# Kernel optimization log

Measured on AMD Instinct MI355X. Metric: run time of the kernel, lower is better.

Reference implementation:

```python
import jax, jax.numpy as jnp
import numpy as np

B, T, I, H, L, O = 256, 2048, 64, 128, 2, 10


def setup_inputs() -> dict:
    key = jax.random.key(0)
    ks = jax.random.split(key, 12)
    s_i = 1.0 / np.sqrt(H)  # torch RNN init scale
    inp = {"x": jax.random.normal(ks[0], (B, T, I), dtype=jnp.float32)}
    in_sizes = [I, H]
    for l in range(L):
        inp[f"W_ih_{l}"] = jax.random.uniform(ks[1 + 4 * l], (3 * H, in_sizes[l]), minval=-s_i, maxval=s_i)
        inp[f"W_hh_{l}"] = jax.random.uniform(ks[2 + 4 * l], (3 * H, H), minval=-s_i, maxval=s_i)
        inp[f"b_ih_{l}"] = jax.random.uniform(ks[3 + 4 * l], (3 * H,), minval=-s_i, maxval=s_i)
        inp[f"b_hh_{l}"] = jax.random.uniform(ks[4 + 4 * l], (3 * H,), minval=-s_i, maxval=s_i)
    s_o = 1.0 / np.sqrt(H)
    inp["fc_W"] = jax.random.uniform(ks[9], (O, H), minval=-s_o, maxval=s_o)
    inp["fc_b"] = jax.random.uniform(ks[10], (O,), minval=-s_o, maxval=s_o)
    return inp


def gru_layer(x_seq, W_ih, W_hh, b_ih, b_hh):
    # x_seq: [B, T, D_in] -> hs: [B, T, H]. PyTorch GRU gate order: r, z, n.
    b, t, _ = x_seq.shape
    h = W_hh.shape[1]
    gates_x = jnp.einsum('bti,gi->btg', x_seq, W_ih) + b_ih  # [B, T, 3H], precomputed

    def step(h_prev, gx):
        gh = h_prev @ W_hh.T + b_hh  # [B, 3H]
        xr, xz, xn = jnp.split(gx, 3, axis=-1)
        hr, hz, hn = jnp.split(gh, 3, axis=-1)
        r = jax.nn.sigmoid(xr + hr)
        z = jax.nn.sigmoid(xz + hz)
        n = jnp.tanh(xn + r * hn)
        h_new = (1.0 - z) * n + z * h_prev
        return h_new, h_new

    h0 = jnp.zeros((b, h), dtype=x_seq.dtype)
    _, hs = jax.lax.scan(step, h0, jnp.swapaxes(gates_x, 0, 1))  # time-major scan
    return jnp.swapaxes(hs, 0, 1)


def reference(x, W_ih_0, W_hh_0, b_ih_0, b_hh_0, W_ih_1, W_hh_1, b_ih_1, b_hh_1, fc_W, fc_b):
    out = gru_layer(x, W_ih_0, W_hh_0, b_ih_0, b_hh_0)
    out = gru_layer(out, W_ih_1, W_hh_1, b_ih_1, b_hh_1)
    return out[:, -1, :] @ fc_W.T + fc_b  # [B, O]
```

## Files before the change

### kernel.cpp

```cpp
#include <hip/hip_runtime.h>
#include <hip/hip_bf16.h>

#define B_ 256
#define T_ 2048
#define I_ 64
#define H_ 128
#define G_ 384
#define O_ 10

typedef _Float16 half2_t __attribute__((ext_vector_type(2)));
typedef _Float16 half8_t __attribute__((ext_vector_type(8)));

__device__ __forceinline__ float sigm_(float s) {
  s = fminf(fmaxf(s, -30.f), 30.f);
  return __builtin_amdgcn_rcpf(1.f + __expf(-s));
}
__device__ __forceinline__ float tanh_(float s) {
  s = fminf(fmaxf(s, -15.f), 15.f);
  return 1.f - 2.f * __builtin_amdgcn_rcpf(1.f + __expf(2.f * s));
}

#define LOADW(DST, SRC) do { const float* s_ = (SRC); half8_t w_; \
  w_[0]=(_Float16)s_[0]; w_[1]=(_Float16)s_[1]; w_[2]=(_Float16)s_[2]; w_[3]=(_Float16)s_[3]; \
  w_[4]=(_Float16)s_[4]; w_[5]=(_Float16)s_[5]; w_[6]=(_Float16)s_[6]; w_[7]=(_Float16)s_[7]; \
  (DST) = w_; } while(0)

#define D8(S0,S1,S2,S3,W,XV) do { half8_t xv_ = (XV); half8_t w_ = (W); \
  S0 = __builtin_amdgcn_fdot2(__builtin_shufflevector(w_,w_,0,1), __builtin_shufflevector(xv_,xv_,0,1), (S0), false); \
  S1 = __builtin_amdgcn_fdot2(__builtin_shufflevector(w_,w_,2,3), __builtin_shufflevector(xv_,xv_,2,3), (S1), false); \
  S2 = __builtin_amdgcn_fdot2(__builtin_shufflevector(w_,w_,4,5), __builtin_shufflevector(xv_,xv_,4,5), (S2), false); \
  S3 = __builtin_amdgcn_fdot2(__builtin_shufflevector(w_,w_,6,7), __builtin_shufflevector(xv_,xv_,6,7), (S3), false); \
} while(0)

__global__ __launch_bounds__(768, 3) void gru_net(
    const float* __restrict__ x,
    const float* __restrict__ Wih0, const float* __restrict__ Whh0,
    const float* __restrict__ bih0, const float* __restrict__ bhh0,
    const float* __restrict__ Wih1, const float* __restrict__ Whh1,
    const float* __restrict__ bih1, const float* __restrict__ bhh1,
    const float* __restrict__ fcW, const float* __restrict__ fcb,
    float* __restrict__ out)
{
  const int b   = blockIdx.x;
  const int tid = threadIdx.x;

  __shared__ alignas(16) half2_t xp[2][I_/2];
  __shared__ alignas(16) half2_t h0p[2][H_/2];
  __shared__ alignas(16) half2_t h1p[2][H_/2];
  __shared__ float h0f[H_], h1f[H_];
  __shared__ float rz0[2*H_], rz1[2*H_];

  const size_t xbase = (size_t)b * T_ * I_;

  if (tid < H_) { h0f[tid] = 0.f; h1f[tid] = 0.f; }
  if (tid < H_/2) {
    half2_t z2; z2[0] = (_Float16)0.f; z2[1] = (_Float16)0.f;
    h0p[0][tid] = z2; h0p[1][tid] = z2;
    h1p[0][tid] = z2; h1p[1][tid] = z2;
  }
  if (tid < I_) {
    ((_Float16*)xp[0])[tid] = (_Float16)x[xbase + tid];
  }
  __syncthreads();

  const bool r0 = (tid < G_);
  const int  g  = r0 ? tid : tid - G_;

  half8_t a0{},a1{},a2{},a3{},a4{},a5{},a6{},a7{},
          a8{},a9{},a10{},a11{},a12{},a13{},a14{},a15{};
  half8_t w0{},w1{},w2{},w3{},w4{},w5{},w6{},w7{},
          w8{},w9{},w10{},w11{},w12{},w13{},w14{},w15{};
  float bi, bh;
  if (r0) {
    const float* p0 = Wih0 + (size_t)g * I_;
    LOADW(a0,p0+ 0); LOADW(a1,p0+ 8); LOADW(a2,p0+16); LOADW(a3,p0+24);
    LOADW(a4,p0+32); LOADW(a5,p0+40); LOADW(a6,p0+48); LOADW(a7,p0+56);
    const float* p1 = Whh0 + (size_t)g * H_;
    LOADW(w0 ,p1+  0); LOADW(w1 ,p1+  8); LOADW(w2 ,p1+ 16); LOADW(w3 ,p1+ 24);
    LOADW(w4 ,p1+ 32); LOADW(w5 ,p1+ 40); LOADW(w6 ,p1+ 48); LOADW(w7 ,p1+ 56);
    LOADW(w8 ,p1+ 64); LOADW(w9 ,p1+ 72); LOADW(w10,p1+ 80); LOADW(w11,p1+ 88);
    LOADW(w12,p1+ 96); LOADW(w13,p1+104); LOADW(w14,p1+112); LOADW(w15,p1+120);
    bi = bih0[g]; bh = bhh0[g];
  } else {
    const float* p0 = Wih1 + (size_t)g * H_;
    LOADW(a0 ,p0+  0); LOADW(a1 ,p0+  8); LOADW(a2 ,p0+ 16); LOADW(a3 ,p0+ 24);
    LOADW(a4 ,p0+ 32); LOADW(a5 ,p0+ 40); LOADW(a6 ,p0+ 48); LOADW(a7 ,p0+ 56);
    LOADW(a8 ,p0+ 64); LOADW(a9 ,p0+ 72); LOADW(a10,p0+ 80); LOADW(a11,p0+ 88);
    LOADW(a12,p0+ 96); LOADW(a13,p0+104); LOADW(a14,p0+112); LOADW(a15,p0+120);
    const float* p1 = Whh1 + (size_t)g * H_;
    LOADW(w0 ,p1+  0); LOADW(w1 ,p1+  8); LOADW(w2 ,p1+ 16); LOADW(w3 ,p1+ 24);
    LOADW(w4 ,p1+ 32); LOADW(w5 ,p1+ 40); LOADW(w6 ,p1+ 48); LOADW(w7 ,p1+ 56);
    LOADW(w8 ,p1+ 64); LOADW(w9 ,p1+ 72); LOADW(w10,p1+ 80); LOADW(w11,p1+ 88);
    LOADW(w12,p1+ 96); LOADW(w13,p1+104); LOADW(w14,p1+112); LOADW(w15,p1+120);
    bi = bih1[g]; bh = bhh1[g];
  }

  float* rzW = r0 ? rz0 : rz1;
  float* hfW = r0 ? h0f : h1f;
  _Float16* hpW0 = (_Float16*)(r0 ? h0p[0] : h1p[0]);
  _Float16* hpW1 = (_Float16*)(r0 ? h0p[1] : h1p[1]);

  for (int p = 0; p <= T_; ++p) {
    float ax = 0.f, ah = 0.f, xnext = 0.f;
    const bool act = r0 ? (p < T_) : (p >= 1);
    if (act) {
      const half8_t* hA = (const half8_t*)h0p[(p & 1) ^ 1];
      float s0=0.f, s1=0.f, s2=0.f, s3=0.f;
      float c0=0.f, c1=0.f, c2=0.f, c3=0.f;
      if (r0) {
        if (g < I_ && p + 1 < T_) xnext = x[xbase + (size_t)(p + 1) * I_ + g];
        const half8_t* xr = (const half8_t*)xp[p & 1];
        D8(s0,s1,s2,s3, a0, xr[0]); D8(s0,s1,s2,s3, a1, xr[1]);
        D8(s0,s1,s2,s3, a2, xr[2]); D8(s0,s1,s2,s3, a3, xr[3]);
        D8(s0,s1,s2,s3, a4, xr[4]); D8(s0,s1,s2,s3, a5, xr[5]);
        D8(s0,s1,s2,s3, a6, xr[6]); D8(s0,s1,s2,s3, a7, xr[7]);
        D8(c0,c1,c2,c3, w0 , hA[ 0]); D8(c0,c1,c2,c3, w1 , hA[ 1]);
        D8(c0,c1,c2,c3, w2 , hA[ 2]); D8(c0,c1,c2,c3, w3 , hA[ 3]);
        D8(c0,c1,c2,c3, w4 , hA[ 4]); D8(c0,c1,c2,c3, w5 , hA[ 5]);
        D8(c0,c1,c2,c3, w6 , hA[ 6]); D8(c0,c1,c2,c3, w7 , hA[ 7]);
        D8(c0,c1,c2,c3, w8 , hA[ 8]); D8(c0,c1,c2,c3, w9 , hA[ 9]);
        D8(c0,c1,c2,c3, w10, hA[10]); D8(c0,c1,c2,c3, w11, hA[11]);
        D8(c0,c1,c2,c3, w12, hA[12]); D8(c0,c1,c2,c3, w13, hA[13]);
        D8(c0,c1,c2,c3, w14, hA[14]); D8(c0,c1,c2,c3, w15, hA[15]);
      } else {
        const half8_t* h1r = (const half8_t*)h1p[(p & 1) ^ 1];
        D8(s0,s1,s2,s3, a0 , hA[ 0]); D8(s0,s1,s2,s3, a1 , hA[ 1]);
        D8(s0,s1,s2,s3, a2 , hA[ 2]); D8(s0,s1,s2,s3, a3 , hA[ 3]);
        D8(s0,s1,s2,s3, a4 , hA[ 4]); D8(s0,s1,s2,s3, a5 , hA[ 5]);
        D8(s0,s1,s2,s3, a6 , hA[ 6]); D8(s0,s1,s2,s3, a7 , hA[ 7]);
        D8(s0,s1,s2,s3, a8 , hA[ 8]); D8(s0,s1,s2,s3, a9 , hA[ 9]);
        D8(s0,s1,s2,s3, a10, hA[10]); D8(s0,s1,s2,s3, a11, hA[11]);
        D8(s0,s1,s2,s3, a12, hA[12]); D8(s0,s1,s2,s3, a13, hA[13]);
        D8(s0,s1,s2,s3, a14, hA[14]); D8(s0,s1,s2,s3, a15, hA[15]);
        D8(c0,c1,c2,c3, w0 , h1r[ 0]); D8(c0,c1,c2,c3, w1 , h1r[ 1]);
        D8(c0,c1,c2,c3, w2 , h1r[ 2]); D8(c0,c1,c2,c3, w3 , h1r[ 3]);
        D8(c0,c1,c2,c3, w4 , h1r[ 4]); D8(c0,c1,c2,c3, w5 , h1r[ 5]);
        D8(c0,c1,c2,c3, w6 , h1r[ 6]); D8(c0,c1,c2,c3, w7 , h1r[ 7]);
        D8(c0,c1,c2,c3, w8 , h1r[ 8]); D8(c0,c1,c2,c3, w9 , h1r[ 9]);
        D8(c0,c1,c2,c3, w10, h1r[10]); D8(c0,c1,c2,c3, w11, h1r[11]);
        D8(c0,c1,c2,c3, w12, h1r[12]); D8(c0,c1,c2,c3, w13, h1r[13]);
        D8(c0,c1,c2,c3, w14, h1r[14]); D8(c0,c1,c2,c3, w15, h1r[15]);
      }
      ax = bi + ((s0 + s1) + (s2 + s3));
      ah = bh + ((c0 + c1) + (c2 + c3));
      if (g < 2*H_) rzW[g] = sigm_(ax + ah);
    }
    __syncthreads();
    if (act) {
      if (g >= 2*H_) {
        const int j = g - 2*H_;
        const float r = rzW[j], z = rzW[H_ + j];
        const float n = tanh_(ax + r * ah);
        const float hn = z * (hfW[j] - n) + n;
        hfW[j] = hn;
        ((p & 1) ? hpW1 : hpW0)[j] = (_Float16)hn;
      }
      if (r0 && g < I_ && p + 1 < T_)
        ((_Float16*)xp[(p + 1) & 1])[g] = (_Float16)xnext;
    }
    __syncthreads();
  }

  if (tid < O_) {
    float acc = fcb[tid];
    const float* wr = fcW + (size_t)tid * H_;
    for (int k = 0; k < H_; ++k) acc = fmaf(h1f[k], wr[k], acc);
    out[(size_t)b * O_ + tid] = acc;
  }
}

extern "C" void kernel_launch(void* const* d_in, const int* in_sizes, int n_in,
                              void* d_out, int out_size, void* d_ws, size_t ws_size,
                              hipStream_t stream) {
  const float* x    = (const float*)d_in[0];
  const float* Wih0 = (const float*)d_in[1];
  const float* Whh0 = (const float*)d_in[2];
  const float* bih0 = (const float*)d_in[3];
  const float* bhh0 = (const float*)d_in[4];
  const float* Wih1 = (const float*)d_in[5];
  const float* Whh1 = (const float*)d_in[6];
  const float* bih1 = (const float*)d_in[7];
  const float* bhh1 = (const float*)d_in[8];
  const float* fcW  = (const float*)d_in[9];
  const float* fcb  = (const float*)d_in[10];

  gru_net<<<dim3(B_), dim3(768), 0, stream>>>(
      x, Wih0, Whh0, bih0, bhh0, Wih1, Whh1, bih1, bhh1, fcW, fcb,
      (float*)d_out);
}
```

Baseline: 2.564 ms.

## Split GRU into per-layer kernels with 8-lane gate reduction and async x prefetch

Replaces the fused two-layer wavefront kernel with two kernels: layer 0 writes its fp16 hidden sequence to workspace and layer 1 streams it back. Each kernel uses 1024 threads, with 8 lanes per hidden unit splitting the dot products and combining them through DPP reductions. This removes one of the two barriers per step. Inputs are prefetched several steps ahead with global_load_lds, and the activation functions drop their clamps and use exp2. The cost is an extra round trip through global memory (about 128 MB written then read), losing the overlap between layers, and a fallback path when the workspace is too small.

```diff
diff --git a/kernel.cpp b/kernel.cpp
--- a/kernel.cpp
+++ b/kernel.cpp
@@ -7,23 +7,209 @@
 #define H_ 128
 #define G_ 384
 #define O_ 10
+#define WS_NEED ((size_t)B_ * (size_t)T_ * (size_t)H_ * 2u)
 
 typedef _Float16 half2_t __attribute__((ext_vector_type(2)));
 typedef _Float16 half8_t __attribute__((ext_vector_type(8)));
 
 __device__ __forceinline__ float sigm_(float s) {
-  s = fminf(fmaxf(s, -30.f), 30.f);
-  return __builtin_amdgcn_rcpf(1.f + __expf(-s));
+  float e = __builtin_amdgcn_exp2f(s * -1.44269504f);
+  return __builtin_amdgcn_rcpf(1.f + e);
 }
 __device__ __forceinline__ float tanh_(float s) {
-  s = fminf(fmaxf(s, -15.f), 15.f);
-  return 1.f - 2.f * __builtin_amdgcn_rcpf(1.f + __expf(2.f * s));
-}
-
-#define LOADW(DST, SRC) do { const float* s_ = (SRC); half8_t w_; \
+  float e = __builtin_amdgcn_exp2f(s * 2.88539009f);
+  return 1.f - 2.f * __builtin_amdgcn_rcpf(1.f + e);
+}
+
+__device__ __forceinline__ float octsum_(float v) {
+  int t;
+  t = __builtin_amdgcn_update_dpp(0, __builtin_bit_cast(int, v), 0xB1, 0xF, 0xF, true);
+  v += __builtin_bit_cast(float, t);
+  t = __builtin_amdgcn_update_dpp(0, __builtin_bit_cast(int, v), 0x4E, 0xF, 0xF, true);
+  v += __builtin_bit_cast(float, t);
+  t = __builtin_amdgcn_update_dpp(0, __builtin_bit_cast(int, v), 0x141, 0xF, 0xF, true);
+  v += __builtin_bit_cast(float, t);
+  return v;
+}
+
+#define CVT8(DST, SRC) do { const float* s_ = (SRC); half8_t w_; \
   w_[0]=(_Float16)s_[0]; w_[1]=(_Float16)s_[1]; w_[2]=(_Float16)s_[2]; w_[3]=(_Float16)s_[3]; \
   w_[4]=(_Float16)s_[4]; w_[5]=(_Float16)s_[5]; w_[6]=(_Float16)s_[6]; w_[7]=(_Float16)s_[7]; \
   (DST) = w_; } while(0)
+
+__device__ __forceinline__ float dot8h(half8_t w, half8_t v, float acc) {
+  acc = __builtin_amdgcn_fdot2(__builtin_shufflevector(w,w,0,1), __builtin_shufflevector(v,v,0,1), acc, false);
+  acc = __builtin_amdgcn_fdot2(__builtin_shufflevector(w,w,2,3), __builtin_shufflevector(v,v,2,3), acc, false);
+  acc = __builtin_amdgcn_fdot2(__builtin_shufflevector(w,w,4,5), __builtin_shufflevector(v,v,4,5), acc, false);
+  acc = __builtin_amdgcn_fdot2(__builtin_shufflevector(w,w,6,7), __builtin_shufflevector(v,v,6,7), acc, false);
+  return acc;
+}
+__device__ __forceinline__ float dot4f(float4 w, float4 v, float acc) {
+  acc = fmaf(w.x, v.x, acc); acc = fmaf(w.y, v.y, acc);
+  acc = fmaf(w.z, v.z, acc); acc = fmaf(w.w, v.w, acc);
+  return acc;
+}
+
+__global__ __launch_bounds__(1024, 4)
+__attribute__((amdgpu_waves_per_eu(4, 4)))
+void gru_l0(const float* __restrict__ x,
+            const float* __restrict__ Wih, const float* __restrict__ Whh,
+            const float* __restrict__ bih, const float* __restrict__ bhh,
+            ushort* __restrict__ wsh)
+{
+  const int b = blockIdx.x, tid = threadIdx.x;
+  const int j = tid >> 3, s = tid & 7;
+
+  __shared__ alignas(16) float  xst[4][I_];
+  __shared__ alignas(16) ushort h0p[2][H_];
+
+  float4 wxr_a, wxr_b, wxz_a, wxz_b, wxn_a, wxn_b;
+  half8_t whr_a, whr_b, whz_a, whz_b, whn_a, whn_b;
+  {
+    const float* p;
+    p = Wih + (size_t)j * I_ + s * 8;            wxr_a = *(const float4*)p; wxr_b = *(const float4*)(p + 4);
+    p = Wih + (size_t)(H_ + j) * I_ + s * 8;     wxz_a = *(const float4*)p; wxz_b = *(const float4*)(p + 4);
+    p = Wih + (size_t)(2*H_ + j) * I_ + s * 8;   wxn_a = *(const float4*)p; wxn_b = *(const float4*)(p + 4);
+    p = Whh + (size_t)j * H_ + s * 16;           CVT8(whr_a, p); CVT8(whr_b, p + 8);
+    p = Whh + (size_t)(H_ + j) * H_ + s * 16;    CVT8(whz_a, p); CVT8(whz_b, p + 8);
+    p = Whh + (size_t)(2*H_ + j) * H_ + s * 16;  CVT8(whn_a, p); CVT8(whn_b, p + 8);
+  }
+  const float br  = bih[j] + bhh[j];
+  const float bz  = bih[H_ + j] + bhh[H_ + j];
+  const float bin = bih[2*H_ + j], bhn = bhh[2*H_ + j];
+
+  const size_t xrow = (size_t)b * T_;
+  float hprev = 0.f;
+
+  if (tid < H_) h0p[0][tid] = 0;
+  if (tid < 16) {
+    __builtin_amdgcn_global_load_lds(x + (xrow + 0) * I_ + tid * 4, &xst[0][0], 16, 0, 0);
+    __builtin_amdgcn_global_load_lds(x + (xrow + 1) * I_ + tid * 4, &xst[1][0], 16, 0, 0);
+    __builtin_amdgcn_global_load_lds(x + (xrow + 2) * I_ + tid * 4, &xst[2][0], 16, 0, 0);
+  }
+  if (tid < 64) { asm volatile("s_waitcnt vmcnt(0)" ::: "memory"); }
+  __syncthreads();
+
+  for (int t = 0; t < T_; ++t) {
+    if (tid < 16) {
+      int tt = t + 3; if (tt > T_ - 1) tt = T_ - 1;
+      __builtin_amdgcn_global_load_lds(x + (xrow + tt) * I_ + tid * 4,
+                                       &xst[(t + 3) & 3][0], 16, 0, 0);
+    }
+    const float4*  xr = (const float4*)&xst[t & 3][s * 8];
+    const float4   xa = xr[0], xb = xr[1];
+    const half8_t* hr = (const half8_t*)&h0p[t & 1][s * 16];
+    const half8_t  ha = hr[0], hb = hr[1];
+
+    float accr = dot4f(wxr_a, xa, dot4f(wxr_b, xb, 0.f));
+    float accz = dot4f(wxz_a, xa, dot4f(wxz_b, xb, 0.f));
+    float axn  = dot4f(wxn_a, xa, dot4f(wxn_b, xb, 0.f));
+    accr = dot8h(whr_a, ha, dot8h(whr_b, hb, accr));
+    accz = dot8h(whz_a, ha, dot8h(whz_b, hb, accz));
+    float ahn  = dot8h(whn_a, ha, dot8h(whn_b, hb, 0.f));
+
+    const float vr = octsum_(accr), vz = octsum_(accz);
+    const float an = octsum_(axn),  hn_ = octsum_(ahn);
+
+    const float r = sigm_(vr + br);
+    const float z = sigm_(vz + bz);
+    const float n = tanh_(fmaf(r, hn_ + bhn, an + bin));
+    const float hnew = fmaf(z, hprev - n, n);
+    hprev = hnew;
+
+    if (s == 0) {
+      const ushort hbits = __builtin_bit_cast(ushort, (_Float16)hnew);
+      h0p[(t + 1) & 1][j] = hbits;
+      wsh[(xrow + t) * H_ + j] = hbits;
+    }
+    if (tid < 64) { asm volatile("s_waitcnt vmcnt(3)" ::: "memory"); }
+    __syncthreads();
+  }
+}
+
+__global__ __launch_bounds__(1024, 4)
+__attribute__((amdgpu_waves_per_eu(4, 4)))
+void gru_l1(const ushort* __restrict__ wsh,
+            const float* __restrict__ Wih, const float* __restrict__ Whh,
+            const float* __restrict__ bih, const float* __restrict__ bhh,
+            const float* __restrict__ fcW, const float* __restrict__ fcb,
+            float* __restrict__ out)
+{
+  const int b = blockIdx.x, tid = threadIdx.x;
+  const int j = tid >> 3, s = tid & 7;
+
+  __shared__ alignas(16) ushort h0st[4][H_];
+  __shared__ alignas(16) ushort h1p[2][H_];
+  __shared__ float hfin[H_];
+
+  half8_t wir_a, wir_b, wiz_a, wiz_b, win_a, win_b;
+  half8_t whr_a, whr_b, whz_a, whz_b, whn_a, whn_b;
+  {
+    const float* p;
+    p = Wih + (size_t)j * H_ + s * 16;           CVT8(wir_a, p); CVT8(wir_b, p + 8);
+    p = Wih + (size_t)(H_ + j) * H_ + s * 16;    CVT8(wiz_a, p); CVT8(wiz_b, p + 8);
+    p = Wih + (size_t)(2*H_ + j) * H_ + s * 16;  CVT8(win_a, p); CVT8(win_b, p + 8);
+    p = Whh + (size_t)j * H_ + s * 16;           CVT8(whr_a, p); CVT8(whr_b, p + 8);
+    p = Whh + (size_t)(H_ + j) * H_ + s * 16;    CVT8(whz_a, p); CVT8(whz_b, p + 8);
+    p = Whh + (size_t)(2*H_ + j) * H_ + s * 16;  CVT8(whn_a, p); CVT8(whn_b, p + 8);
+  }
+  const float br  = bih[j] + bhh[j];
+  const float bz  = bih[H_ + j] + bhh[H_ + j];
+  const float bin = bih[2*H_ + j], bhn = bhh[2*H_ + j];
+
+  const size_t hrow = (size_t)b * T_;
+  float hprev = 0.f;
+
+  if (tid < H_) h1p[0][tid] = 0;
+  if (tid < 16) {
+    __builtin_amdgcn_global_load_lds(wsh + (hrow + 0) * H_ + tid * 8, &h0st[0][0], 16, 0, 0);
+    __builtin_amdgcn_global_load_lds(wsh + (hrow + 1) * H_ + tid * 8, &h0st[1][0], 16, 0, 0);
+    __builtin_amdgcn_global_load_lds(wsh + (hrow + 2) * H_ + tid * 8, &h0st[2][0], 16, 0, 0);
+  }
+  if (tid < 64) { asm volatile("s_waitcnt vmcnt(0)" ::: "memory"); }
+  __syncthreads();
+
+  for (int t = 0; t < T_; ++t) {
+    if (tid < 16) {
+      int tt = t + 3; if (tt > T_ - 1) tt = T_ - 1;
+      __builtin_amdgcn_global_load_lds(wsh + (hrow + tt) * H_ + tid * 8,
+                                       &h0st[(t + 3) & 3][0], 16, 0, 0);
+    }
+    const half8_t* ar = (const half8_t*)&h0st[t & 3][s * 16];
+    const half8_t  aa = ar[0], ab = ar[1];
+    const half8_t* hr = (const half8_t*)&h1p[t & 1][s * 16];
+    const half8_t  ha = hr[0], hb = hr[1];
+
+    float accr = dot8h(wir_a, aa, dot8h(wir_b, ab, 0.f));
+    float accz = dot8h(wiz_a, aa, dot8h(wiz_b, ab, 0.f));
+    float axn  = dot8h(win_a, aa, dot8h(win_b, ab, 0.f));
+    accr = dot8h(whr_a, ha, dot8h(whr_b, hb, accr));
+    accz = dot8h(whz_a, ha, dot8h(whz_b, hb, accz));
+    float ahn  = dot8h(whn_a, ha, dot8h(whn_b, hb, 0.f));
+
+    const float vr = octsum_(accr), vz = octsum_(accz);
+    const float an = octsum_(axn),  hn_ = octsum_(ahn);
+
+    const float r = sigm_(vr + br);
+    const float z = sigm_(vz + bz);
+    const float n = tanh_(fmaf(r, hn_ + bhn, an + bin));
+    const float hnew = fmaf(z, hprev - n, n);
+    hprev = hnew;
+
+    if (s == 0) h1p[(t + 1) & 1][j] = __builtin_bit_cast(ushort, (_Float16)hnew);
+    if (tid < 64) { asm volatile("s_waitcnt vmcnt(2)" ::: "memory"); }
+    __syncthreads();
+  }
+
+  if (s == 0) hfin[j] = hprev;
+  __syncthreads();
+  if (tid < O_) {
+    float a = fcb[tid];
+    const float* wr = fcW + (size_t)tid * H_;
+    for (int k = 0; k < H_; ++k) a = fmaf(wr[k], hfin[k], a);
+    out[(size_t)b * O_ + tid] = a;
+  }
+}
 
 #define D8(S0,S1,S2,S3,W,XV) do { half8_t xv_ = (XV); half8_t w_ = (W); \
   S0 = __builtin_amdgcn_fdot2(__builtin_shufflevector(w_,w_,0,1), __builtin_shufflevector(xv_,xv_,0,1), (S0), false); \
@@ -31,6 +217,15 @@
   S2 = __builtin_amdgcn_fdot2(__builtin_shufflevector(w_,w_,4,5), __builtin_shufflevector(xv_,xv_,4,5), (S2), false); \
   S3 = __builtin_amdgcn_fdot2(__builtin_shufflevector(w_,w_,6,7), __builtin_shufflevector(xv_,xv_,6,7), (S3), false); \
 } while(0)
+
+__device__ __forceinline__ float sigm2_(float s) {
+  s = fminf(fmaxf(s, -30.f), 30.f);
+  return __builtin_amdgcn_rcpf(1.f + __expf(-s));
+}
+__device__ __forceinline__ float tanh2_(float s) {
+  s = fminf(fmaxf(s, -15.f), 15.f);
+  return 1.f - 2.f * __builtin_amdgcn_rcpf(1.f + __expf(2.f * s));
+}
 
 __global__ __launch_bounds__(768, 3) void gru_net(
     const float* __restrict__ x,
@@ -58,9 +253,7 @@
     h0p[0][tid] = z2; h0p[1][tid] = z2;
     h1p[0][tid] = z2; h1p[1][tid] = z2;
   }
-  if (tid < I_) {
-    ((_Float16*)xp[0])[tid] = (_Float16)x[xbase + tid];
-  }
+  if (tid < I_) ((_Float16*)xp[0])[tid] = (_Float16)x[xbase + tid];
   __syncthreads();
 
   const bool r0 = (tid < G_);
@@ -73,25 +266,25 @@
   float bi, bh;
   if (r0) {
     const float* p0 = Wih0 + (size_t)g * I_;
-    LOADW(a0,p0+ 0); LOADW(a1,p0+ 8); LOADW(a2,p0+16); LOADW(a3,p0+24);
-    LOADW(a4,p0+32); LOADW(a5,p0+40); LOADW(a6,p0+48); LOADW(a7,p0+56);
+    CVT8(a0,p0+ 0); CVT8(a1,p0+ 8); CVT8(a2,p0+16); CVT8(a3,p0+24);
+    CVT8(a4,p0+32); CVT8(a5,p0+40); CVT8(a6,p0+48); CVT8(a7,p0+56);
     const float* p1 = Whh0 + (size_t)g * H_;
-    LOADW(w0 ,p1+  0); LOADW(w1 ,p1+  8); LOADW(w2 ,p1+ 16); LOADW(w3 ,p1+ 24);
-    LOADW(w4 ,p1+ 32); LOADW(w5 ,p1+ 40); LOADW(w6 ,p1+ 48); LOADW(w7 ,p1+ 56);
-    LOADW(w8 ,p1+ 64); LOADW(w9 ,p1+ 72); LOADW(w10,p1+ 80); LOADW(w11,p1+ 88);
-    LOADW(w12,p1+ 96); LOADW(w13,p1+104); LOADW(w14,p1+112); LOADW(w15,p1+120);
+    CVT8(w0 ,p1+  0); CVT8(w1 ,p1+  8); CVT8(w2 ,p1+ 16); CVT8(w3 ,p1+ 24);
+    CVT8(w4 ,p1+ 32); CVT8(w5 ,p1+ 40); CVT8(w6 ,p1+ 48); CVT8(w7 ,p1+ 56);
+    CVT8(w8 ,p1+ 64); CVT8(w9 ,p1+ 72); CVT8(w10,p1+ 80); CVT8(w11,p1+ 88);
+    CVT8(w12,p1+ 96); CVT8(w13,p1+104); CVT8(w14,p1+112); CVT8(w15,p1+120);
     bi = bih0[g]; bh = bhh0[g];
   } else {
     const float* p0 = Wih1 + (size_t)g * H_;
-    LOADW(a0 ,p0+  0); LOADW(a1 ,p0+  8); LOADW(a2 ,p0+ 16); LOADW(a3 ,p0+ 24);
-    LOADW(a4 ,p0+ 32); LOADW(a5 ,p0+ 40); LOADW(a6 ,p0+ 48); LOADW(a7 ,p0+ 56);
-    LOADW(a8 ,p0+ 64); LOADW(a9 ,p0+ 72); LOADW(a10,p0+ 80); LOADW(a11,p0+ 88);
-    LOADW(a12,p0+ 96); LOADW(a13,p0+104); LOADW(a14,p0+112); LOADW(a15,p0+120);
+    CVT8(a0 ,p0+  0); CVT8(a1 ,p0+  8); CVT8(a2 ,p0+ 16); CVT8(a3 ,p0+ 24);
+    CVT8(a4 ,p0+ 32); CVT8(a5 ,p0+ 40); CVT8(a6 ,p0+ 48); CVT8(a7 ,p0+ 56);
+    CVT8(a8 ,p0+ 64); CVT8(a9 ,p0+ 72); CVT8(a10,p0+ 80); CVT8(a11,p0+ 88);
+    CVT8(a12,p0+ 96); CVT8(a13,p0+104); CVT8(a14,p0+112); CVT8(a15,p0+120);
     const float* p1 = Whh1 + (size_t)g * H_;
-    LOADW(w0 ,p1+  0); LOADW(w1 ,p1+  8); LOADW(w2 ,p1+ 16); LOADW(w3 ,p1+ 24);
-    LOADW(w4 ,p1+ 32); LOADW(w5 ,p1+ 40); LOADW(w6 ,p1+ 48); LOADW(w7 ,p1+ 56);
-    LOADW(w8 ,p1+ 64); LOADW(w9 ,p1+ 72); LOADW(w10,p1+ 80); LOADW(w11,p1+ 88);
-    LOADW(w12,p1+ 96); LOADW(w13,p1+104); LOADW(w14,p1+112); LOADW(w15,p1+120);
+    CVT8(w0 ,p1+  0); CVT8(w1 ,p1+  8); CVT8(w2 ,p1+ 16); CVT8(w3 ,p1+ 24);
+    CVT8(w4 ,p1+ 32); CVT8(w5 ,p1+ 40); CVT8(w6 ,p1+ 48); CVT8(w7 ,p1+ 56);
+    CVT8(w8 ,p1+ 64); CVT8(w9 ,p1+ 72); CVT8(w10,p1+ 80); CVT8(w11,p1+ 88);
+    CVT8(w12,p1+ 96); CVT8(w13,p1+104); CVT8(w14,p1+112); CVT8(w15,p1+120);
     bi = bih1[g]; bh = bhh1[g];
   }
 
@@ -143,17 +336,17 @@
       }
       ax = bi + ((s0 + s1) + (s2 + s3));
       ah = bh + ((c0 + c1) + (c2 + c3));
-      if (g < 2*H_) rzW[g] = sigm_(ax + ah);
+      if (g < 2*H_) rzW[g] = sigm2_(ax + ah);
     }
     __syncthreads();
     if (act) {
       if (g >= 2*H_) {
-        const int j = g - 2*H_;
-        const float r = rzW[j], z = rzW[H_ + j];
-        const float n = tanh_(ax + r * ah);
-        const float hn = z * (hfW[j] - n) + n;
-        hfW[j] = hn;
-        ((p & 1) ? hpW1 : hpW0)[j] = (_Float16)hn;
+        const int jj = g - 2*H_;
+        const float r = rzW[jj], z = rzW[H_ + jj];
+        const float n = tanh2_(ax + r * ah);
+        const float hn = z * (hfW[jj] - n) + n;
+        hfW[jj] = hn;
+        ((p & 1) ? hpW1 : hpW0)[jj] = (_Float16)hn;
       }
       if (r0 && g < I_ && p + 1 < T_)
         ((_Float16*)xp[(p + 1) & 1])[g] = (_Float16)xnext;
@@ -184,7 +377,14 @@
   const float* fcW  = (const float*)d_in[9];
   const float* fcb  = (const float*)d_in[10];
 
-  gru_net<<<dim3(B_), dim3(768), 0, stream>>>(
-      x, Wih0, Whh0, bih0, bhh0, Wih1, Whh1, bih1, bhh1, fcW, fcb,
-      (float*)d_out);
-}
+  if (ws_size >= WS_NEED) {
+    ushort* wsh = (ushort*)d_ws;
+    gru_l0<<<dim3(B_), dim3(1024), 0, stream>>>(x, Wih0, Whh0, bih0, bhh0, wsh);
+    gru_l1<<<dim3(B_), dim3(1024), 0, stream>>>(wsh, Wih1, Whh1, bih1, bhh1,
+                                                fcW, fcb, (float*)d_out);
+  } else {
+    gru_net<<<dim3(B_), dim3(768), 0, stream>>>(
+        x, Wih0, Whh0, bih0, bhh0, Wih1, Whh1, bih1, bhh1, fcW, fcb,
+        (float*)d_out);
+  }
+}
```

Measured after the change: 3.155 ms. +23.0%, slower.
